# Optimization experiments

Measured on AMD Instinct MI355X. Metric: run time of the kernel, lower is better.

The kernel has to match this reference:

```python
import jax, jax.numpy as jnp
import numpy as np

N_QUBITS = 10
N_LAYERS = 3


def _apply_1q(state, gate, q, batched):
    # state: (B,) + (2,)*n ; gate: (2,2) or (B,2,2)
    s = jnp.moveaxis(state, q + 1, -1)
    shp = s.shape
    s = s.reshape(shp[0], -1, 2)
    eq = 'bij,brj->bri' if batched else 'ij,brj->bri'
    s = jnp.einsum(eq, gate, s).reshape(shp)
    return jnp.moveaxis(s, -1, q + 1)


def _apply_cnot(state, c, t):
    s = jnp.moveaxis(state, (c + 1, t + 1), (-2, -1))
    s = s.at[..., 1, :].set(s[..., 1, ::-1])  # flip target where control==1
    return jnp.moveaxis(s, (-2, -1), (c + 1, t + 1))


def _rot_gate(phi, theta, omega):
    # PennyLane Rot(phi,theta,omega) = RZ(omega) @ RY(theta) @ RZ(phi)
    ch = jnp.cos(theta * 0.5).astype(jnp.complex64)
    sh = jnp.sin(theta * 0.5).astype(jnp.complex64)
    m00 = jnp.exp(-1j * (phi + omega) * 0.5) * ch
    m01 = -jnp.exp(1j * (phi - omega) * 0.5) * sh
    m10 = jnp.exp(-1j * (phi - omega) * 0.5) * sh
    m11 = jnp.exp(1j * (phi + omega) * 0.5) * ch
    return jnp.stack([jnp.stack([m00, m01]), jnp.stack([m10, m11])])


def _circuit(x, weights):
    B = x.shape[0]
    n = N_QUBITS
    state = jnp.zeros((B,) + (2,) * n, jnp.complex64)
    state = state.at[(slice(None),) + (0,) * n].set(1.0)  # |0...0>
    c = jnp.cos(x * 0.5)  # (B, n)
    s = jnp.sin(x * 0.5)
    for l in range(N_LAYERS):
        # AngleEmbedding: RY(x_q) on each wire (batched gates)
        for q in range(n):
            g = jnp.stack([jnp.stack([c[:, q], -s[:, q]], -1),
                           jnp.stack([s[:, q], c[:, q]], -1)], -2).astype(jnp.complex64)
            state = _apply_1q(state, g, q, True)
        # StronglyEntanglingLayers, single sub-layer: Rot on each wire
        for q in range(n):
            g = _rot_gate(weights[l, q, 0], weights[l, q, 1], weights[l, q, 2])
            state = _apply_1q(state, g, q, False)
        # ring of CNOTs with range r=1
        for q in range(n):
            state = _apply_cnot(state, q, (q + 1) % n)
    probs = jnp.abs(state) ** 2  # (B,) + (2,)*n, real
    outs = []
    for q in range(n):
        axes = tuple(a for a in range(1, n + 1) if a != q + 1)
        m = probs.sum(axis=axes)  # (B, 2)
        outs.append(m[:, 0] - m[:, 1])  # <Z_q>
    return jnp.stack(outs, axis=1).astype(jnp.float32)


def setup_inputs() -> dict:
    key = jax.random.key(0)
    k1, k2 = jax.random.split(key)
    x = jax.random.normal(k1, (4096, N_QUBITS), dtype=jnp.float32)
    weights = jax.random.uniform(k2, (N_LAYERS, N_QUBITS, 3), dtype=jnp.float32,
                                 minval=-np.pi, maxval=np.pi)
    return {"x": x, "weights": weights}


def reference(x, weights):
    return _circuit(x, weights)
```

## Files before the change

kernel.cpp:

```cpp
#include <hip/hip_runtime.h>

#define NQ 10
#define NL 3

typedef float v2f __attribute__((ext_vector_type(2)));

__device__ __forceinline__ int   f2i(float v) { union { float f; int i; } u; u.f = v; return u.i; }
__device__ __forceinline__ float i2f(int v)   { union { int i; float f; } u; u.i = v; return u.f; }

__device__ __forceinline__ v2f cmul(v2f a, v2f b) {
    return (v2f){ fmaf(a.x, b.x, -a.y * b.y), fmaf(a.x, b.y, a.y * b.x) };
}

template<int C> __device__ __forceinline__ int dppm(int v) {
    return __builtin_amdgcn_mov_dpp(v, C, 0xF, 0xF, false);
}

template<int LM>
__device__ __forceinline__ v2f xlane(v2f v, int baddr) {
    if constexpr (LM == 0) return v;
    int x = f2i(v.x), y = f2i(v.y);
    if constexpr (LM == 1)       { x = dppm<177>(x); y = dppm<177>(y); }
    else if constexpr (LM == 2)  { x = dppm<78>(x);  y = dppm<78>(y); }
    else if constexpr (LM == 3)  { x = dppm<27>(x);  y = dppm<27>(y); }
    else if constexpr (LM < 32) {
        constexpr int off = (LM << 10) | 0x1F;
        x = __builtin_amdgcn_ds_swizzle(x, off);
        y = __builtin_amdgcn_ds_swizzle(y, off);
    } else {
        x = __builtin_amdgcn_ds_bpermute(baddr, x);
        y = __builtin_amdgcn_ds_bpermute(baddr, y);
    }
    return (v2f){ i2f(x), i2f(y) };
}

template<int MASK, int RMASK>
__device__ __forceinline__ void apply_gate(v2f (&a)[16], float4 r0, float4 r1,
                                           float cq, float sq, int lane)
{
    constexpr int LM = (MASK >> 4) & 63;
    constexpr int JM = MASK & 15;
    constexpr int RH = (RMASK >> 4) & 63;
    constexpr int RL = RMASK & 15;

    const float g00r = fmaf(r0.x, cq,  r0.z * sq), g00i = fmaf(r0.y, cq,  r0.w * sq);
    const float g01r = fmaf(r0.z, cq, -r0.x * sq), g01i = fmaf(r0.w, cq, -r0.y * sq);
    const float g10r = fmaf(r1.x, cq,  r1.z * sq), g10i = fmaf(r1.y, cq,  r1.w * sq);
    const float g11r = fmaf(r1.z, cq, -r1.x * sq), g11i = fmaf(r1.w, cq, -r1.y * sq);

    const bool lp = (RH != 0) && (__popc(lane & RH) & 1);
    const float A0r = lp ? g11r : g00r, A0i = lp ? g11i : g00i;
    const float B0r = lp ? g10r : g01r, B0i = lp ? g10i : g01i;
    const float A1r = lp ? g00r : g11r, A1i = lp ? g00i : g11i;
    const float B1r = lp ? g01r : g10r, B1i = lp ? g01i : g10i;

    const int baddr = ((lane ^ LM) << 2);

    v2f o[16];
    #pragma unroll
    for (int j = 0; j < 16; ++j) o[j] = xlane<LM>(a[j ^ JM], baddr);

#define QNN_F(J) { constexpr int SP_ = __builtin_popcount((J) & RL) & 1;      \
    const float Ar = SP_ ? A1r : A0r, Ai = SP_ ? A1i : A0i;                   \
    const float Br = SP_ ? B1r : B0r, Bi = SP_ ? B1i : B0i;                   \
    const float ar = a[J].x, ai = a[J].y, pr = o[J].x, pi = o[J].y;           \
    float re = ar * Ar;       re = fmaf(-Ai, ai, re);                         \
    re = fmaf(Br, pr, re);    re = fmaf(-Bi, pi, re);                         \
    float im = ai * Ar;       im = fmaf(Ai, ar, im);                          \
    im = fmaf(Br, pi, im);    im = fmaf(Bi, pr, im);                          \
    a[J] = (v2f){re, im}; }
    QNN_F(0) QNN_F(1) QNN_F(2) QNN_F(3) QNN_F(4) QNN_F(5) QNN_F(6) QNN_F(7)
    QNN_F(8) QNN_F(9) QNN_F(10) QNN_F(11) QNN_F(12) QNN_F(13) QNN_F(14) QNN_F(15)
#undef QNN_F
}

__global__ __launch_bounds__(256, 4)
void qnn_kernel(const float* __restrict__ x, const float* __restrict__ w,
                float* __restrict__ out)
{
    __shared__ float4 rotL[NL * NQ][2];

    const int t    = threadIdx.x;
    const int lane = t & 63;
    const int b    = blockIdx.x * 4 + (t >> 6);

    if (t < NL * NQ) {
        const float* wp = w + t * 3;
        float phi = wp[0], th = wp[1], om = wp[2];
        float ct = cosf(th * 0.5f), st = sinf(th * 0.5f);
        float ap = (phi + om) * 0.5f, am = (phi - om) * 0.5f;
        float cap = cosf(ap), sap = sinf(ap);
        float cam = cosf(am), sam = sinf(am);
        rotL[t][0] = make_float4(cap * ct, -sap * ct, -cam * st, -sam * st);
        rotL[t][1] = make_float4(cam * st, -sam * st,  cap * ct,  sap * ct);
    }
    __syncthreads();

    const float* xb = x + (size_t)__builtin_amdgcn_readfirstlane(b * NQ);
    float c_[NQ], s_[NQ];
    #pragma unroll
    for (int q = 0; q < NQ; ++q) {
        float xv = xb[q] * 0.5f;
        c_[q] = i2f(__builtin_amdgcn_readfirstlane(f2i(__cosf(xv))));
        s_[q] = i2f(__builtin_amdgcn_readfirstlane(f2i(__sinf(xv))));
    }

    v2f c0[4], c1[4];
    v2f Ln = {1.f, 0.f};
    #pragma unroll
    for (int q = 0; q < NQ; ++q) {
        float4 r0 = rotL[q][0], r1 = rotL[q][1];
        float cq = c_[q], sq = s_[q];
        v2f g0 = { fmaf(r0.x, cq, r0.z * sq), fmaf(r0.y, cq, r0.w * sq) };
        v2f g1 = { fmaf(r1.x, cq, r1.z * sq), fmaf(r1.y, cq, r1.w * sq) };
        if (q < 4) { c0[q] = g0; c1[q] = g1; }
        else {
            v2f gg = ((lane >> (q - 4)) & 1) ? g1 : g0;
            Ln = (q == 4) ? gg : cmul(Ln, gg);
        }
    }
    v2f S01[4], SH[4];
    #pragma unroll
    for (int j = 0; j < 4; ++j)
        S01[j] = cmul((j & 1) ? c1[0] : c0[0], (j & 2) ? c1[1] : c0[1]);
    #pragma unroll
    for (int h = 0; h < 4; ++h)
        SH[h] = cmul(cmul((h & 1) ? c1[2] : c0[2], (h & 2) ? c1[3] : c0[3]), Ln);
    v2f a[16];
    #pragma unroll
    for (int j = 0; j < 16; ++j)
        a[j] = cmul(S01[j & 3], SH[j >> 2]);

#define GATE(IDX, Q, MASK, RMASK) \
    apply_gate<MASK, RMASK>(a, rotL[IDX][0], rotL[IDX][1], c_[Q], s_[Q], lane);
    GATE(10, 0, 0x003, 0x3FE)  GATE(11, 1, 0x006, 0x003)
    GATE(12, 2, 0x00C, 0x007)  GATE(13, 3, 0x018, 0x00F)
    GATE(14, 4, 0x030, 0x01F)  GATE(15, 5, 0x060, 0x03F)
    GATE(16, 6, 0x0C0, 0x07F)  GATE(17, 7, 0x180, 0x0FF)
    GATE(18, 8, 0x300, 0x1FF)  GATE(19, 9, 0x203, 0x3FF)
    GATE(20, 0, 0x005, 0x2AB)  GATE(21, 1, 0x00A, 0x3FD)
    GATE(22, 2, 0x014, 0x3FA)  GATE(23, 3, 0x028, 0x3F5)
    GATE(24, 4, 0x050, 0x3EA)  GATE(25, 5, 0x0A0, 0x3D5)
    GATE(26, 6, 0x140, 0x3AA)  GATE(27, 7, 0x280, 0x355)
    GATE(28, 8, 0x103, 0x2AA)  GATE(29, 9, 0x206, 0x155)
#undef GATE

    float P[16];
    #pragma unroll
    for (int j = 0; j < 16; ++j)
        P[j] = fmaf(a[j].x, a[j].x, a[j].y * a[j].y);
    #pragma unroll
    for (int bit = 0; bit < 4; ++bit) {
        #pragma unroll
        for (int j = 0; j < 16; ++j)
            if (!(j & (1 << bit))) {
                int k = j | (1 << bit);
                float u = P[j], v = P[k];
                P[j] = u + v;
                P[k] = u - v;
            }
    }

    const int bp32 = ((lane ^ 32) << 2);
    float vout = 0.f;
#define MEAS(Q, RM)                                                           \
    { constexpr int RH_ = ((RM) >> 4) & 63;                                   \
      constexpr int RL_ = (RM) & 15;                                          \
      float v = P[RL_];                                                       \
      if (__popc(lane & RH_) & 1) v = -v;                                     \
      v += i2f(dppm<177>(f2i(v)));                                 \
      v += i2f(dppm<78>(f2i(v)));                                  \
      v += i2f(dppm<321>(dppm<27>(f2i(v))));                  \
      v += i2f(dppm<320>(dppm<321>(f2i(v))));                \
      v += i2f(__builtin_amdgcn_ds_swizzle(f2i(v), (16 << 10) | 0x1F));       \
      v += i2f(__builtin_amdgcn_ds_bpermute(bp32, f2i(v)));                   \
      if (lane == (Q)) vout = v; }
    MEAS(0, 0x0CD) MEAS(1, 0x156) MEAS(2, 0x2AC) MEAS(3, 0x159)
    MEAS(4, 0x2B3) MEAS(5, 0x166) MEAS(6, 0x2CC) MEAS(7, 0x199)
    MEAS(8, 0x333) MEAS(9, 0x266)
#undef MEAS

    if (lane < NQ) out[b * NQ + lane] = vout;
}

extern "C" void kernel_launch(void* const* d_in, const int* in_sizes, int n_in,
                              void* d_out, int out_size, void* d_ws, size_t ws_size,
                              hipStream_t stream) {
    const float* x = (const float*)d_in[0];
    const float* w = (const float*)d_in[1];
    float* out = (float*)d_out;
    const int B = in_sizes[0] / NQ;
    qnn_kernel<<<B / 4, 256, 0, stream>>>(x, w, out);
}
```

Baseline: 77.93 us.

## Process two batch samples per wavefront using packed float2 SIMD arithmetic

Each wavefront now simulates two circuits at once. The state is stored as separate real and imaginary v2f arrays, where the x and y components belong to different samples, so the arithmetic can map to packed FP32 instructions (v_pk_fma/v_pk_mul). The grid is halved and launch bounds are relaxed to allow more registers. The cost is doubled register pressure, lower occupancy, and twice as many cross-lane shuffles per wave. Per-gate coefficients are no longer wave-uniform scalars; they become per-sample vectors.

```diff
diff --git a/kernel.cpp b/kernel.cpp
--- a/kernel.cpp
+++ b/kernel.cpp
@@ -7,14 +7,12 @@
 
 __device__ __forceinline__ int   f2i(float v) { union { float f; int i; } u; u.f = v; return u.i; }
 __device__ __forceinline__ float i2f(int v)   { union { int i; float f; } u; u.i = v; return u.f; }
-
-__device__ __forceinline__ v2f cmul(v2f a, v2f b) {
-    return (v2f){ fmaf(a.x, b.x, -a.y * b.y), fmaf(a.x, b.y, a.y * b.x) };
-}
+__device__ __forceinline__ v2f   sp(float f)  { return (v2f){ f, f }; }
 
 template<int C> __device__ __forceinline__ int dppm(int v) {
     return __builtin_amdgcn_mov_dpp(v, C, 0xF, 0xF, false);
 }
+
 
 template<int LM>
 __device__ __forceinline__ v2f xlane(v2f v, int baddr) {
@@ -34,47 +32,59 @@
     return (v2f){ i2f(x), i2f(y) };
 }
 
+struct cpx { v2f re, im; };
+__device__ __forceinline__ cpx cm(cpx a, cpx b) {
+    cpx r;
+    r.re = a.re * b.re - a.im * b.im;
+    r.im = a.re * b.im + a.im * b.re;
+    return r;
+}
+
 template<int MASK, int RMASK>
-__device__ __forceinline__ void apply_gate(v2f (&a)[16], float4 r0, float4 r1,
-                                           float cq, float sq, int lane)
+__device__ __forceinline__ void apply_gate(v2f (&re)[16], v2f (&im)[16],
+                                           float4 r0, float4 r1,
+                                           v2f C, v2f S, int lane)
 {
     constexpr int LM = (MASK >> 4) & 63;
     constexpr int JM = MASK & 15;
     constexpr int RH = (RMASK >> 4) & 63;
     constexpr int RL = RMASK & 15;
 
-    const float g00r = fmaf(r0.x, cq,  r0.z * sq), g00i = fmaf(r0.y, cq,  r0.w * sq);
-    const float g01r = fmaf(r0.z, cq, -r0.x * sq), g01i = fmaf(r0.w, cq, -r0.y * sq);
-    const float g10r = fmaf(r1.x, cq,  r1.z * sq), g10i = fmaf(r1.y, cq,  r1.w * sq);
-    const float g11r = fmaf(r1.z, cq, -r1.x * sq), g11i = fmaf(r1.w, cq, -r1.y * sq);
+    const int baddr = ((lane ^ LM) << 2);
+
+    v2f ore[16], oim[16];
+    #pragma unroll
+    for (int j = 0; j < 16; ++j) ore[j] = xlane<LM>(re[j ^ JM], baddr);
+    #pragma unroll
+    for (int j = 0; j < 16; ++j) oim[j] = xlane<LM>(im[j ^ JM], baddr);
+
+    const v2f G00R = sp(r0.x) * C + sp(r0.z) * S;
+    const v2f G00I = sp(r0.y) * C + sp(r0.w) * S;
+    const v2f G01R = sp(r0.z) * C - sp(r0.x) * S;
+    const v2f G01I = sp(r0.w) * C - sp(r0.y) * S;
+    const v2f G10R = sp(r1.x) * C + sp(r1.z) * S;
+    const v2f G10I = sp(r1.y) * C + sp(r1.w) * S;
+    const v2f G11R = sp(r1.z) * C - sp(r1.x) * S;
+    const v2f G11I = sp(r1.w) * C - sp(r1.y) * S;
 
     const bool lp = (RH != 0) && (__popc(lane & RH) & 1);
-    const float A0r = lp ? g11r : g00r, A0i = lp ? g11i : g00i;
-    const float B0r = lp ? g10r : g01r, B0i = lp ? g10i : g01i;
-    const float A1r = lp ? g00r : g11r, A1i = lp ? g00i : g11i;
-    const float B1r = lp ? g01r : g10r, B1i = lp ? g01i : g10i;
-
-    const int baddr = ((lane ^ LM) << 2);
-
-    v2f o[16];
-    #pragma unroll
-    for (int j = 0; j < 16; ++j) o[j] = xlane<LM>(a[j ^ JM], baddr);
+    const v2f A0R = lp ? G11R : G00R, A0I = lp ? G11I : G00I;
+    const v2f B0R = lp ? G10R : G01R, B0I = lp ? G10I : G01I;
+    const v2f A1R = lp ? G00R : G11R, A1I = lp ? G00I : G11I;
+    const v2f B1R = lp ? G01R : G10R, B1I = lp ? G01I : G10I;
 
 #define QNN_F(J) { constexpr int SP_ = __builtin_popcount((J) & RL) & 1;      \
-    const float Ar = SP_ ? A1r : A0r, Ai = SP_ ? A1i : A0i;                   \
-    const float Br = SP_ ? B1r : B0r, Bi = SP_ ? B1i : B0i;                   \
-    const float ar = a[J].x, ai = a[J].y, pr = o[J].x, pi = o[J].y;           \
-    float re = ar * Ar;       re = fmaf(-Ai, ai, re);                         \
-    re = fmaf(Br, pr, re);    re = fmaf(-Bi, pi, re);                         \
-    float im = ai * Ar;       im = fmaf(Ai, ar, im);                          \
-    im = fmaf(Br, pi, im);    im = fmaf(Bi, pr, im);                          \
-    a[J] = (v2f){re, im}; }
+    const v2f CAR = SP_ ? A1R : A0R, CAI = SP_ ? A1I : A0I;                   \
+    const v2f CBR = SP_ ? B1R : B0R, CBI = SP_ ? B1I : B0I;                   \
+    const v2f ar = re[J], ai = im[J], pr = ore[J], pi = oim[J];               \
+    re[J] = CAR * ar - CAI * ai + CBR * pr - CBI * pi;                        \
+    im[J] = CAR * ai + CAI * ar + CBR * pi + CBI * pr; }
     QNN_F(0) QNN_F(1) QNN_F(2) QNN_F(3) QNN_F(4) QNN_F(5) QNN_F(6) QNN_F(7)
     QNN_F(8) QNN_F(9) QNN_F(10) QNN_F(11) QNN_F(12) QNN_F(13) QNN_F(14) QNN_F(15)
 #undef QNN_F
 }
 
-__global__ __launch_bounds__(256, 4)
+__global__ __launch_bounds__(256, 2)
 void qnn_kernel(const float* __restrict__ x, const float* __restrict__ w,
                 float* __restrict__ out)
 {
@@ -82,7 +92,7 @@
 
     const int t    = threadIdx.x;
     const int lane = t & 63;
-    const int b    = blockIdx.x * 4 + (t >> 6);
+    const int wv   = blockIdx.x * 4 + (t >> 6);
 
     if (t < NL * NQ) {
         const float* wp = w + t * 3;
@@ -96,43 +106,50 @@
     }
     __syncthreads();
 
-    const float* xb = x + (size_t)__builtin_amdgcn_readfirstlane(b * NQ);
-    float c_[NQ], s_[NQ];
+    const float* xb = x + (size_t)(wv * 2 * NQ);
+    v2f C_[NQ], S_[NQ];
     #pragma unroll
     for (int q = 0; q < NQ; ++q) {
-        float xv = xb[q] * 0.5f;
-        c_[q] = i2f(__builtin_amdgcn_readfirstlane(f2i(__cosf(xv))));
-        s_[q] = i2f(__builtin_amdgcn_readfirstlane(f2i(__sinf(xv))));
-    }
-
-    v2f c0[4], c1[4];
-    v2f Ln = {1.f, 0.f};
-    #pragma unroll
-    for (int q = 0; q < NQ; ++q) {
-        float4 r0 = rotL[q][0], r1 = rotL[q][1];
-        float cq = c_[q], sq = s_[q];
-        v2f g0 = { fmaf(r0.x, cq, r0.z * sq), fmaf(r0.y, cq, r0.w * sq) };
-        v2f g1 = { fmaf(r1.x, cq, r1.z * sq), fmaf(r1.y, cq, r1.w * sq) };
-        if (q < 4) { c0[q] = g0; c1[q] = g1; }
-        else {
-            v2f gg = ((lane >> (q - 4)) & 1) ? g1 : g0;
-            Ln = (q == 4) ? gg : cmul(Ln, gg);
+        float x0 = xb[q] * 0.5f, x1 = xb[NQ + q] * 0.5f;
+        C_[q] = (v2f){ __cosf(x0), __cosf(x1) };
+        S_[q] = (v2f){ __sinf(x0), __sinf(x1) };
+    }
+
+    v2f re[16], im[16];
+    {
+        cpx c0[4], c1[4], Ln;
+        #pragma unroll
+        for (int q = 0; q < NQ; ++q) {
+            float4 r0 = rotL[q][0], r1v = rotL[q][1];
+            cpx g0, g1;
+            g0.re = sp(r0.x) * C_[q] + sp(r0.z) * S_[q];
+            g0.im = sp(r0.y) * C_[q] + sp(r0.w) * S_[q];
+            g1.re = sp(r1v.x) * C_[q] + sp(r1v.z) * S_[q];
+            g1.im = sp(r1v.y) * C_[q] + sp(r1v.w) * S_[q];
+            if (q < 4) { c0[q] = g0; c1[q] = g1; }
+            else {
+                const bool bit = (lane >> (q - 4)) & 1;
+                cpx gg; gg.re = bit ? g1.re : g0.re; gg.im = bit ? g1.im : g0.im;
+                Ln = (q == 4) ? gg : cm(Ln, gg);
+            }
         }
-    }
-    v2f S01[4], SH[4];
-    #pragma unroll
-    for (int j = 0; j < 4; ++j)
-        S01[j] = cmul((j & 1) ? c1[0] : c0[0], (j & 2) ? c1[1] : c0[1]);
-    #pragma unroll
-    for (int h = 0; h < 4; ++h)
-        SH[h] = cmul(cmul((h & 1) ? c1[2] : c0[2], (h & 2) ? c1[3] : c0[3]), Ln);
-    v2f a[16];
-    #pragma unroll
-    for (int j = 0; j < 16; ++j)
-        a[j] = cmul(S01[j & 3], SH[j >> 2]);
-
-#define GATE(IDX, Q, MASK, RMASK) \
-    apply_gate<MASK, RMASK>(a, rotL[IDX][0], rotL[IDX][1], c_[Q], s_[Q], lane);
+        cpx S01[4], SH[4];
+        #pragma unroll
+        for (int j = 0; j < 4; ++j)
+            S01[j] = cm((j & 1) ? c1[0] : c0[0], (j & 2) ? c1[1] : c0[1]);
+        #pragma unroll
+        for (int h = 0; h < 4; ++h)
+            SH[h] = cm(cm((h & 1) ? c1[2] : c0[2], (h & 2) ? c1[3] : c0[3]), Ln);
+        #pragma unroll
+        for (int j = 0; j < 16; ++j) {
+            cpx A = cm(S01[j & 3], SH[j >> 2]);
+            re[j] = A.re; im[j] = A.im;
+        }
+    }
+
+#define GATE(IDX, Q, MASK, RMASK)                                             \
+    apply_gate<MASK, RMASK>(re, im, rotL[IDX][0], rotL[IDX][1],               \
+                            C_[Q], S_[Q], lane);
     GATE(10, 0, 0x003, 0x3FE)  GATE(11, 1, 0x006, 0x003)
     GATE(12, 2, 0x00C, 0x007)  GATE(13, 3, 0x018, 0x00F)
     GATE(14, 4, 0x030, 0x01F)  GATE(15, 5, 0x060, 0x03F)
@@ -145,42 +162,56 @@
     GATE(28, 8, 0x103, 0x2AA)  GATE(29, 9, 0x206, 0x155)
 #undef GATE
 
-    float P[16];
+    v2f P[16];
     #pragma unroll
     for (int j = 0; j < 16; ++j)
-        P[j] = fmaf(a[j].x, a[j].x, a[j].y * a[j].y);
+        P[j] = re[j] * re[j] + im[j] * im[j];
     #pragma unroll
     for (int bit = 0; bit < 4; ++bit) {
         #pragma unroll
         for (int j = 0; j < 16; ++j)
             if (!(j & (1 << bit))) {
                 int k = j | (1 << bit);
-                float u = P[j], v = P[k];
+                v2f u = P[j], v = P[k];
                 P[j] = u + v;
                 P[k] = u - v;
             }
     }
 
     const int bp32 = ((lane ^ 32) << 2);
-    float vout = 0.f;
+    v2f vout = {0.f, 0.f};
 #define MEAS(Q, RM)                                                           \
     { constexpr int RH_ = ((RM) >> 4) & 63;                                   \
       constexpr int RL_ = (RM) & 15;                                          \
-      float v = P[RL_];                                                       \
+      v2f v = P[RL_];                                                         \
       if (__popc(lane & RH_) & 1) v = -v;                                     \
-      v += i2f(dppm<177>(f2i(v)));                                 \
-      v += i2f(dppm<78>(f2i(v)));                                  \
-      v += i2f(dppm<321>(dppm<27>(f2i(v))));                  \
-      v += i2f(dppm<320>(dppm<321>(f2i(v))));                \
-      v += i2f(__builtin_amdgcn_ds_swizzle(f2i(v), (16 << 10) | 0x1F));       \
-      v += i2f(__builtin_amdgcn_ds_bpermute(bp32, f2i(v)));                   \
+      v2f tt;                                                                 \
+      tt.x = i2f(dppm<177>(f2i(v.x))); tt.y = i2f(dppm<177>(f2i(v.y)));       \
+      v += tt;                                                     \
+      tt.x = i2f(dppm<78>(f2i(v.x)));  tt.y = i2f(dppm<78>(f2i(v.y)));        \
+      v += tt;                                                     \
+      tt.x = i2f(dppm<321>(dppm<27>(f2i(v.x))));                              \
+      tt.y = i2f(dppm<321>(dppm<27>(f2i(v.y))));                              \
+      v += tt;                                                \
+      tt.x = i2f(dppm<320>(dppm<321>(f2i(v.x))));                             \
+      tt.y = i2f(dppm<320>(dppm<321>(f2i(v.y))));                             \
+      v += tt;                                               \
+      tt.x = i2f(__builtin_amdgcn_ds_swizzle(f2i(v.x), (16 << 10) | 0x1F));   \
+      tt.y = i2f(__builtin_amdgcn_ds_swizzle(f2i(v.y), (16 << 10) | 0x1F));   \
+      v += tt;                                                     \
+      tt.x = i2f(__builtin_amdgcn_ds_bpermute(bp32, f2i(v.x)));               \
+      tt.y = i2f(__builtin_amdgcn_ds_bpermute(bp32, f2i(v.y)));               \
+      v += tt;                                                     \
       if (lane == (Q)) vout = v; }
     MEAS(0, 0x0CD) MEAS(1, 0x156) MEAS(2, 0x2AC) MEAS(3, 0x159)
     MEAS(4, 0x2B3) MEAS(5, 0x166) MEAS(6, 0x2CC) MEAS(7, 0x199)
     MEAS(8, 0x333) MEAS(9, 0x266)
 #undef MEAS
 
-    if (lane < NQ) out[b * NQ + lane] = vout;
+    if (lane < NQ) {
+        out[(wv * 2)     * NQ + lane] = vout.x;
+        out[(wv * 2 + 1) * NQ + lane] = vout.y;
+    }
 }
 
 extern "C" void kernel_launch(void* const* d_in, const int* in_sizes, int n_in,
@@ -190,5 +221,5 @@
     const float* w = (const float*)d_in[1];
     float* out = (float*)d_out;
     const int B = in_sizes[0] / NQ;
-    qnn_kernel<<<B / 4, 256, 0, stream>>>(x, w, out);
-}
+    qnn_kernel<<<B / 8, 256, 0, stream>>>(x, w, out);
+}
```

New measurement: 76.72 us. Within noise of the previous version (-1.6%).
